# Performance work log

Measured on AMD Instinct MI355X. Metric: run time of the kernel, lower is better.

The kernel has to match this reference:

```python
import jax, jax.numpy as jnp
import numpy as np

MP_LAYERS = 3
PROPBETA = 0.05


def setup_inputs() -> dict:
    key = jax.random.key(0)
    k1, k2, k3, k4, k5, k6 = jax.random.split(key, 6)
    B, N, S, D = 32, 64, 336, 32
    x = jax.random.normal(k1, (B, N, S), dtype=jnp.float32)
    adj = jax.random.uniform(k2, (B, S, N, N), dtype=jnp.float32)
    # row-normalize like Graph_constructor output (rows sum to 1)
    adj = adj / jnp.sum(adj, axis=-1, keepdims=True)
    w_start = jax.random.normal(k3, (1, D), dtype=jnp.float32) / jnp.sqrt(1.0)
    b_start = jax.random.normal(k4, (D,), dtype=jnp.float32) * 0.01
    w_mlp = jax.random.normal(k5, ((MP_LAYERS + 1) * D, 1), dtype=jnp.float32) / jnp.sqrt((MP_LAYERS + 1) * D)
    b_mlp = jax.random.normal(k6, (1,), dtype=jnp.float32) * 0.01
    return {"x": x, "adj": adj, "w_start": w_start, "b_start": b_start,
            "w_mlp": w_mlp, "b_mlp": b_mlp}


def reference(x, adj, w_start, b_start, w_mlp, b_mlp):
    # x: [b, n, s]; adj: [b, s, n, m]
    a = jnp.transpose(adj, (0, 2, 3, 1))           # [b, n, m, s]
    xu = x[..., None]                               # [b, n, s, 1]
    h = jnp.einsum('bnsc,cd->bnsd', xu, w_start) + b_start  # startmlp
    out = [h]
    for _ in range(MP_LAYERS):
        conv = jnp.einsum('bnsc,bnms->bmsc', h, a)  # nconv
        h = PROPBETA * xu + (1.0 - PROPBETA) * conv
        out.append(h)
    h = jnp.concatenate(out, axis=-1)               # [b, n, s, (K+1)*d]
    h = jnp.einsum('bnsc,co->bnso', h, w_mlp) + b_mlp
    return h[..., 0]                                # [b, n, s]
```

## Files before the change

### kernel.cpp

```cpp
#include <hip/hip_runtime.h>


#define BB 32
#define NN 64
#define SS 336
#define DD 32
#define BETA 0.05f
#define OMB 0.95f

#define WAITLDS() __asm__ volatile("s_waitcnt lgkmcnt(0)" ::: "memory")

__global__ __launch_bounds__(256) void dgra_collapsed_kernel(
    const float* __restrict__ x, const float* __restrict__ adj,
    const float* __restrict__ w_start, const float* __restrict__ b_start,
    const float* __restrict__ w_mlp, const float* __restrict__ b_mlp,
    float* __restrict__ out)
{
    const int tid  = threadIdx.x;
    const int lane = tid & 63;
    const int w    = tid >> 6;
    const int blk  = blockIdx.x;
    const int b    = blk / (SS / 4);
    const int s4   = blk % (SS / 4);
    const int s    = s4 * 4 + w;

    const int c  = lane & 31;
    const int hi = lane >> 5;

    const float* Ab = adj + (size_t)(b * SS + s) * (NN * NN);
    float2 av[32];
#pragma unroll
    for (int i = 0; i < 32; ++i)
        av[i] = *reinterpret_cast<const float2*>(Ab + (2 * i + hi) * NN + 2 * c);

    const float xv = x[(size_t)(b * NN + lane) * SS + s];

    const float wd = w_start[c];
    const float bd = b_start[c];
    const float m0 = w_mlp[(2 * hi + 0) * DD + c];
    const float m1 = w_mlp[(2 * hi + 1) * DD + c];
    float p0 = wd * m0, q0 = bd * m0, r0 = m0;
    float p1 = wd * m1, q1 = bd * m1, r1 = m1;
#pragma unroll
    for (int mask = 1; mask <= 16; mask <<= 1) {
        p0 += __shfl_xor(p0, mask, 64);  q0 += __shfl_xor(q0, mask, 64);  r0 += __shfl_xor(r0, mask, 64);
        p1 += __shfl_xor(p1, mask, 64);  q1 += __shfl_xor(q1, mask, 64);  r1 += __shfl_xor(r1, mask, 64);
    }
    const float po0 = __shfl_xor(p0, 32, 64), qo0 = __shfl_xor(q0, 32, 64), ro0 = __shfl_xor(r0, 32, 64);
    const float po1 = __shfl_xor(p1, 32, 64), qo1 = __shfl_xor(q1, 32, 64), ro1 = __shfl_xor(r1, 32, 64);
    const bool lo = (hi == 0);
    const float P0 = lo ? p0  : po0, P1 = lo ? p1  : po1, P2 = lo ? po0 : p0, P3 = lo ? po1 : p1;
    const float Q0 = lo ? q0  : qo0, Q1 = lo ? q1  : qo1, Q2 = lo ? qo0 : q0, Q3 = lo ? qo1 : q1;
    const float R1 = lo ? r1  : ro1, R2 = lo ? ro0 : r0,  R3 = lo ? ro1 : r1;

    const float Pp0 = P0 + BETA * (R1 + R2 + R3);
    const float c0  = Q0 + b_mlp[0];
    const float PpA[4] = {Pp0, P1 + BETA * (R2 + R3), P2 + BETA * R3, P3};
    const float QA[4]  = {Q0, Q1, Q2, Q3};

    __shared__ __align__(16) float2 yu[4][NN];
    yu[w][lane] = make_float2(xv, 1.0f);
    WAITLDS();

    const float4 t01 = *reinterpret_cast<const float4*>(&yu[w][2 * c]);
    float acc0 = fmaf(Pp0, t01.x, c0);
    float acc1 = fmaf(Pp0, t01.z, c0);

#pragma unroll
    for (int k = 1; k <= 3; ++k) {
        float ys0 = 0.f, ys1 = 0.f, us0 = 0.f, us1 = 0.f;
#pragma unroll
        for (int i = 0; i < 32; ++i) {
            const float2 t = yu[w][2 * i + hi];
            ys0 = fmaf(av[i].x, t.x, ys0);
            ys1 = fmaf(av[i].y, t.x, ys1);
            us0 = fmaf(av[i].x, t.y, us0);
            us1 = fmaf(av[i].y, t.y, us1);
        }
        ys0 += __shfl_xor(ys0, 32, 64);
        ys1 += __shfl_xor(ys1, 32, 64);
        us0 += __shfl_xor(us0, 32, 64);
        us1 += __shfl_xor(us1, 32, 64);
        ys0 *= OMB; ys1 *= OMB; us0 *= OMB; us1 *= OMB;

        acc0 = fmaf(PpA[k], ys0, fmaf(QA[k], us0, acc0));
        acc1 = fmaf(PpA[k], ys1, fmaf(QA[k], us1, acc1));

        if (k < 3) {
            if (hi == 0)
                *reinterpret_cast<float4*>(&yu[w][2 * c]) = make_float4(ys0, us0, ys1, us1);
            WAITLDS();
        }
    }

    __shared__ __align__(16) float res[NN][4];
    if (hi == 0) {
        res[2 * c + 0][w] = acc0;
        res[2 * c + 1][w] = acc1;
    }
    __syncthreads();
    if (w == 0) {
        const float4 v = *reinterpret_cast<const float4*>(res[lane]);
        *reinterpret_cast<float4*>(&out[(size_t)(b * NN + lane) * SS + s4 * 4]) = v;
    }
}

extern "C" void kernel_launch(void* const* d_in, const int* in_sizes, int n_in,
                              void* d_out, int out_size, void* d_ws, size_t ws_size,
                              hipStream_t stream) {
    const float* x       = (const float*)d_in[0];
    const float* adj     = (const float*)d_in[1];
    const float* w_start = (const float*)d_in[2];
    const float* b_start = (const float*)d_in[3];
    const float* w_mlp   = (const float*)d_in[4];
    const float* b_mlp   = (const float*)d_in[5];
    float* out = (float*)d_out;

    const int grid = BB * (SS / 4);
    dgra_collapsed_kernel<<<grid, 256, 0, stream>>>(x, adj, w_start, b_start, w_mlp, b_mlp, out);
}
```

Measured before the change: 36.03 us.

## Process four timesteps per wavefront with double-buffered adjacency register prefetch

Each block now has a single 64-thread wavefront that walks four consecutive timesteps. The adjacency tile for the next timestep is loaded into a second register buffer while the current one is being computed, so load latency overlaps with compute inside the wave. The change also drops the shared-memory result transpose and the block barrier, writing float4 outputs directly from registers. In exchange, register pressure doubles (two 64-float buffers), which may lower occupancy, and there are four times fewer waves available to hide latency across the chip.

```diff
diff --git a/kernel.cpp b/kernel.cpp
--- a/kernel.cpp
+++ b/kernel.cpp
@@ -10,37 +10,37 @@
 
 #define WAITLDS() __asm__ volatile("s_waitcnt lgkmcnt(0)" ::: "memory")
 
-__global__ __launch_bounds__(256) void dgra_collapsed_kernel(
+__global__ __launch_bounds__(64) void dgra_pipe2_kernel(
     const float* __restrict__ x, const float* __restrict__ adj,
     const float* __restrict__ w_start, const float* __restrict__ b_start,
     const float* __restrict__ w_mlp, const float* __restrict__ b_mlp,
     float* __restrict__ out)
 {
-    const int tid  = threadIdx.x;
-    const int lane = tid & 63;
-    const int w    = tid >> 6;
-    const int blk  = blockIdx.x;
-    const int b    = blk / (SS / 4);
-    const int s4   = blk % (SS / 4);
-    const int s    = s4 * 4 + w;
+    const int lane = threadIdx.x;
+    const int b    = blockIdx.x / (SS / 4);
+    const int s4   = blockIdx.x % (SS / 4);
+    const int s0   = s4 * 4;
+    const int c    = lane & 31;
+    const int hi   = lane >> 5;
 
-    const int c  = lane & 31;
-    const int hi = lane >> 5;
+    const float wd  = w_start[c];
+    const float bd  = b_start[c];
+    const float m0f = w_mlp[(2 * hi + 0) * DD + c];
+    const float m1f = w_mlp[(2 * hi + 1) * DD + c];
+    const float bm  = b_mlp[0];
 
-    const float* Ab = adj + (size_t)(b * SS + s) * (NN * NN);
-    float2 av[32];
+    const float* Ab = adj + (size_t)(b * SS + s0) * (NN * NN);
+
+    float2 avA[32], avB[32];
 #pragma unroll
     for (int i = 0; i < 32; ++i)
-        av[i] = *reinterpret_cast<const float2*>(Ab + (2 * i + hi) * NN + 2 * c);
+        avA[i] = *reinterpret_cast<const float2*>(Ab + (2 * i + hi) * NN + 2 * c);
 
-    const float xv = x[(size_t)(b * NN + lane) * SS + s];
+    const float4 xq = *reinterpret_cast<const float4*>(&x[(size_t)(b * NN + lane) * SS + s0]);
+    const float xj[4] = {xq.x, xq.y, xq.z, xq.w};
 
-    const float wd = w_start[c];
-    const float bd = b_start[c];
-    const float m0 = w_mlp[(2 * hi + 0) * DD + c];
-    const float m1 = w_mlp[(2 * hi + 1) * DD + c];
-    float p0 = wd * m0, q0 = bd * m0, r0 = m0;
-    float p1 = wd * m1, q1 = bd * m1, r1 = m1;
+    float p0 = wd * m0f, q0 = bd * m0f, r0 = m0f;
+    float p1 = wd * m1f, q1 = bd * m1f, r1 = m1f;
 #pragma unroll
     for (int mask = 1; mask <= 16; mask <<= 1) {
         p0 += __shfl_xor(p0, mask, 64);  q0 += __shfl_xor(q0, mask, 64);  r0 += __shfl_xor(r0, mask, 64);
@@ -52,57 +52,65 @@
     const float P0 = lo ? p0  : po0, P1 = lo ? p1  : po1, P2 = lo ? po0 : p0, P3 = lo ? po1 : p1;
     const float Q0 = lo ? q0  : qo0, Q1 = lo ? q1  : qo1, Q2 = lo ? qo0 : q0, Q3 = lo ? qo1 : q1;
     const float R1 = lo ? r1  : ro1, R2 = lo ? ro0 : r0,  R3 = lo ? ro1 : r1;
+    const float PpA[4] = {P0 + BETA * (R1 + R2 + R3), P1 + BETA * (R2 + R3), P2 + BETA * R3, P3};
+    const float QA[4]  = {Q0, Q1, Q2, Q3};
+    const float c0f = Q0 + bm;
 
-    const float Pp0 = P0 + BETA * (R1 + R2 + R3);
-    const float c0  = Q0 + b_mlp[0];
-    const float PpA[4] = {Pp0, P1 + BETA * (R2 + R3), P2 + BETA * R3, P3};
-    const float QA[4]  = {Q0, Q1, Q2, Q3};
+    __shared__ __align__(16) float2 yu[NN];
+    float r0a[4], r1a[4];
 
-    __shared__ __align__(16) float2 yu[4][NN];
-    yu[w][lane] = make_float2(xv, 1.0f);
-    WAITLDS();
+#define LOADT(DST, T)                                                          \
+    { const float* Abt = Ab + (T) * (NN * NN);                                 \
+      _Pragma("unroll")                                                        \
+      for (int i = 0; i < 32; ++i)                                             \
+          DST[i] = *reinterpret_cast<const float2*>(Abt + (2 * i + hi) * NN + 2 * c); }
 
-    const float4 t01 = *reinterpret_cast<const float4*>(&yu[w][2 * c]);
-    float acc0 = fmaf(Pp0, t01.x, c0);
-    float acc1 = fmaf(Pp0, t01.z, c0);
+#define TASK(CUR, JJ)                                                          \
+    { yu[lane] = make_float2(xj[JJ], 1.0f);                                    \
+      WAITLDS();                                                               \
+      const float4 t01 = *reinterpret_cast<const float4*>(&yu[2 * c]);         \
+      float a0 = fmaf(PpA[0], t01.x, c0f);                                     \
+      float a1 = fmaf(PpA[0], t01.z, c0f);                                     \
+      _Pragma("unroll")                                                        \
+      for (int k = 1; k <= 3; ++k) {                                           \
+          float ys0 = 0.f, ys1 = 0.f, us0 = 0.f, us1 = 0.f;                    \
+          _Pragma("unroll")                                                    \
+          for (int i = 0; i < 32; ++i) {                                       \
+              const float2 t = yu[2 * i + hi];                                 \
+              ys0 = fmaf(CUR[i].x, t.x, ys0);                                  \
+              ys1 = fmaf(CUR[i].y, t.x, ys1);                                  \
+              us0 = fmaf(CUR[i].x, t.y, us0);                                  \
+              us1 = fmaf(CUR[i].y, t.y, us1);                                  \
+          }                                                                    \
+          ys0 += __shfl_xor(ys0, 32, 64);  ys1 += __shfl_xor(ys1, 32, 64);     \
+          us0 += __shfl_xor(us0, 32, 64);  us1 += __shfl_xor(us1, 32, 64);     \
+          ys0 *= OMB; ys1 *= OMB; us0 *= OMB; us1 *= OMB;                      \
+          a0 = fmaf(PpA[k], ys0, fmaf(QA[k], us0, a0));                        \
+          a1 = fmaf(PpA[k], ys1, fmaf(QA[k], us1, a1));                        \
+          if (k < 3) {                                                         \
+              if (hi == 0)                                                     \
+                  *reinterpret_cast<float4*>(&yu[2 * c]) =                     \
+                      make_float4(ys0, us0, ys1, us1);                         \
+              WAITLDS();                                                       \
+          }                                                                    \
+      }                                                                        \
+      r0a[JJ] = a0; r1a[JJ] = a1; }
 
-#pragma unroll
-    for (int k = 1; k <= 3; ++k) {
-        float ys0 = 0.f, ys1 = 0.f, us0 = 0.f, us1 = 0.f;
-#pragma unroll
-        for (int i = 0; i < 32; ++i) {
-            const float2 t = yu[w][2 * i + hi];
-            ys0 = fmaf(av[i].x, t.x, ys0);
-            ys1 = fmaf(av[i].y, t.x, ys1);
-            us0 = fmaf(av[i].x, t.y, us0);
-            us1 = fmaf(av[i].y, t.y, us1);
-        }
-        ys0 += __shfl_xor(ys0, 32, 64);
-        ys1 += __shfl_xor(ys1, 32, 64);
-        us0 += __shfl_xor(us0, 32, 64);
-        us1 += __shfl_xor(us1, 32, 64);
-        ys0 *= OMB; ys1 *= OMB; us0 *= OMB; us1 *= OMB;
+    LOADT(avB, 1);  TASK(avA, 0);
+    LOADT(avA, 2);  TASK(avB, 1);
+    LOADT(avB, 3);  TASK(avA, 2);
+                    TASK(avB, 3);
 
-        acc0 = fmaf(PpA[k], ys0, fmaf(QA[k], us0, acc0));
-        acc1 = fmaf(PpA[k], ys1, fmaf(QA[k], us1, acc1));
+#undef LOADT
+#undef TASK
 
-        if (k < 3) {
-            if (hi == 0)
-                *reinterpret_cast<float4*>(&yu[w][2 * c]) = make_float4(ys0, us0, ys1, us1);
-            WAITLDS();
-        }
-    }
-
-    __shared__ __align__(16) float res[NN][4];
-    if (hi == 0) {
-        res[2 * c + 0][w] = acc0;
-        res[2 * c + 1][w] = acc1;
-    }
-    __syncthreads();
-    if (w == 0) {
-        const float4 v = *reinterpret_cast<const float4*>(res[lane]);
-        *reinterpret_cast<float4*>(&out[(size_t)(b * NN + lane) * SS + s4 * 4]) = v;
-    }
+    const int n = 2 * c + hi;
+    float4 o;
+    o.x = hi ? r1a[0] : r0a[0];
+    o.y = hi ? r1a[1] : r0a[1];
+    o.z = hi ? r1a[2] : r0a[2];
+    o.w = hi ? r1a[3] : r0a[3];
+    *reinterpret_cast<float4*>(&out[(size_t)(b * NN + n) * SS + s0]) = o;
 }
 
 extern "C" void kernel_launch(void* const* d_in, const int* in_sizes, int n_in,
@@ -117,5 +125,5 @@
     float* out = (float*)d_out;
 
     const int grid = BB * (SS / 4);
-    dgra_collapsed_kernel<<<grid, 256, 0, stream>>>(x, adj, w_start, b_start, w_mlp, b_mlp, out);
+    dgra_pipe2_kernel<<<grid, 64, 0, stream>>>(x, adj, w_start, b_start, w_mlp, b_mlp, out);
 }
```

Measured after the change: 41.71 us. 15.8% more time.
